# Performance work log

Measured on AMD Instinct MI355X. Metric: run time of the kernel, lower is better.

Reference implementation:

```python
import jax, jax.numpy as jnp
import numpy as np

B, S1, S2, S3, I, O = 4, 64, 64, 64, 32, 32
MX, MZ = 16, 16
HID = O * 2  # factor=2 feedforward hidden


def setup_inputs() -> dict:
    key = jax.random.key(0)
    ks = jax.random.split(key, 5)
    x = jax.random.normal(ks[0], (B, S1, S2, S3, I), jnp.float32)
    # xavier-normal-ish scale for complex fourier weights stored as [...,2]
    sw = np.float32(np.sqrt(2.0 / (I + O)))
    wx = jax.random.normal(ks[1], (I, O, MX, 2), jnp.float32) * sw
    wz = jax.random.normal(ks[2], (I, O, MZ, 2), jnp.float32) * sw
    w1 = jax.random.normal(ks[3], (O, HID), jnp.float32) * np.float32(np.sqrt(1.0 / O))
    b1 = jnp.zeros((HID,), jnp.float32)
    w2 = jax.random.normal(ks[4], (HID, O), jnp.float32) * np.float32(np.sqrt(1.0 / HID))
    b2 = jnp.zeros((O,), jnp.float32)
    return {"x": x, "wx": wx, "wz": wz, "w1": w1, "b1": b1, "w2": w2, "b2": b2}


def _forward_fourier(x, wx, wz):
    # x: [b, i, s1, s2, s3]
    # z-axis branch
    cwz = wz[..., 0] + 1j * wz[..., 1]          # [i, o, mz] complex
    xfz = jnp.fft.rfft(x, axis=-1, norm='ortho')  # [b,i,s1,s2,S3//2+1]
    pz = jnp.einsum('bixyz,ioz->boxyz', xfz[..., :MZ], cwz)
    pz = jnp.pad(pz, ((0, 0), (0, 0), (0, 0), (0, 0), (0, S3 // 2 + 1 - MZ)))
    xz = jnp.fft.irfft(pz, n=S3, axis=-1, norm='ortho')
    # x-axis branch (note: modes_y branch contributes 0 in the source, xy=0.0)
    cwx = wx[..., 0] + 1j * wx[..., 1]          # [i, o, mx]
    xfx = jnp.fft.rfft(x, axis=2, norm='ortho')  # [b,i,S1//2+1,s2,s3]
    px = jnp.einsum('bixyz,iox->boxyz', xfx[:, :, :MX], cwx)
    px = jnp.pad(px, ((0, 0), (0, 0), (0, S1 // 2 + 1 - MX), (0, 0), (0, 0)))
    xx = jnp.fft.irfft(px, n=S1, axis=2, norm='ortho')
    return xx + xz


def reference(x, wx, wz, w1, b1, w2, b2):
    xt = jnp.transpose(x, (0, 4, 1, 2, 3))      # b i s1 s2 s3
    y = _forward_fourier(xt, wx, wz)
    y = jnp.transpose(y, (0, 2, 3, 4, 1))       # b s1 s2 s3 o
    # backcast FeedForward: Linear -> ReLU -> Linear (dropout=0, no norms)
    h = jax.nn.relu(y @ w1 + b1)
    b_out = h @ w2 + b2
    return b_out
```

## Files before the change

### kernel.cpp

```cpp
#include <hip/hip_runtime.h>

namespace {

typedef _Float16 half_t;
typedef half_t f16x2 __attribute__((ext_vector_type(2)));
typedef half_t f16x8 __attribute__((ext_vector_type(8)));
typedef float f32x4 __attribute__((ext_vector_type(4)));

constexpr size_t RSTR = 64 * 64 * 32;

constexpr int WS_TF = 0;
constexpr int WS_TI = 2048;
constexpr int WS_WZ = 4096;
constexpr int WS_WX = 69632;
constexpr int WS_W1 = 135168;
constexpr int WS_W2 = 137216;

__device__ __forceinline__ float f4get(const float4& v, int u) {
  return u == 0 ? v.x : (u == 1 ? v.y : (u == 2 ? v.z : v.w));
}

__device__ __forceinline__ f32x4 mfma16(f16x8 a, f16x8 b, f32x4 c) {
  return __builtin_amdgcn_mfma_f32_16x16x32_f16(a, b, c, 0, 0, 0);
}

__global__ __launch_bounds__(256) void kinit(const float* __restrict__ wx,
                                             const float* __restrict__ wz,
                                             const float* __restrict__ w1,
                                             const float* __restrict__ w2,
                                             half_t* __restrict__ wsh) {
  const int id = blockIdx.x * 256 + threadIdx.x;
  const int l = id & 63, r = l & 15, g = l >> 4;
  f16x8 frag;
  if (id < 256) {
    int fid = id >> 6, mt = fid >> 1, kt = fid & 1;
#pragma unroll
    for (int e = 0; e < 8; ++e) {
      int k = kt * 32 + 8 * g + e;
      int mc = mt * 16 + r, m = mc >> 1, p = mc & 1;
      float s, c;
      sincospif((float)(m * k) * (1.0f / 32.0f), &s, &c);
      frag[e] = (half_t)(0.125f * (p ? -s : c));
    }
    *(f16x8*)(wsh + WS_TF + (size_t)id * 8) = frag;
  } else if (id < 512) {
    int id2 = id - 256, mt = id2 >> 6;
#pragma unroll
    for (int e = 0; e < 8; ++e) {
      int zp = mt * 16 + r;
      int k = 8 * g + e, m = k >> 1, p = k & 1;
      float s, c;
      sincospif((float)(m * zp) * (1.0f / 32.0f), &s, &c);
      float sc = (m == 0) ? 0.125f : 0.25f;
      frag[e] = (half_t)(p ? -sc * s : sc * c);
    }
    *(f16x8*)(wsh + WS_TI + (size_t)id2 * 8) = frag;
  } else if (id < 16896) {
    int id2 = id - 512;
    const float* wsrc = wz;
    size_t off = WS_WZ;
    if (id2 >= 8192) { id2 -= 8192; wsrc = wx; off = WS_WX; }
    int fid = id2 >> 6, m = fid >> 3, kt = (fid >> 2) & 1, nt = fid & 3;
#pragma unroll
    for (int e = 0; e < 8; ++e) {
      int k = kt * 32 + 8 * g + e, i = k >> 1, p = k & 1;
      int n = nt * 16 + r, o = n >> 1, q = n & 1;
      int base = ((i * 32 + o) * 16 + m) * 2;
      float re = wsrc[base], im = wsrc[base + 1];
      frag[e] = (half_t)(q ? (p ? re : im) : (p ? -im : re));
    }
    *(f16x8*)(wsh + off + (size_t)id2 * 8) = frag;
  } else if (id < 17152) {
    int id2 = id - 16896, nt = id2 >> 6;
#pragma unroll
    for (int e = 0; e < 8; ++e) {
      int k = 8 * g + e, n = nt * 16 + r;
      frag[e] = (half_t)w1[k * 64 + n];
    }
    *(f16x8*)(wsh + WS_W1 + (size_t)id2 * 8) = frag;
  } else if (id < 17408) {
    int id2 = id - 17152, fid = id2 >> 6, kt = fid >> 1, nt = fid & 1;
#pragma unroll
    for (int e = 0; e < 8; ++e) {
      int k = kt * 32 + 8 * g + e, n = nt * 16 + r;
      frag[e] = (half_t)w2[k * 32 + n];
    }
    *(f16x8*)(wsh + WS_W2 + (size_t)id2 * 8) = frag;
  }
}

template <int BR>
__global__ __launch_bounds__(256) void kspec(const float* __restrict__ x,
                                             const half_t* __restrict__ wsh,
                                             const float* __restrict__ b1g,
                                             const float* __restrict__ b2g,
                                             float* __restrict__ outf) {
  __shared__ __align__(16) char smraw[49152];
  half_t* XB = (half_t*)smraw;
  half_t* FB = (half_t*)smraw;
  half_t* PB = (half_t*)(smraw + 32768);
  half_t* outh = (half_t*)outf;
  const int t = threadIdx.x, l = t & 63, w = t >> 6, r = l & 15, g = l >> 4;
  const f32x4 vzero = {0.f, 0.f, 0.f, 0.f};

  const int col0 = blockIdx.x * 8;
  size_t xbase = (size_t)col0 * 2048, zstr = 32, cstr = 2048;

  {
    int c = t >> 5, sub = t & 31;
    int i4 = (sub & 7) * 4, zq = sub >> 3;
    const float* xp = x + xbase + (size_t)c * cstr + i4;
#pragma unroll
    for (int zo = 0; zo < 2; ++zo) {
      int zb = zq * 16 + zo * 8;
      float4 v[8];
#pragma unroll
      for (int zz = 0; zz < 8; ++zz)
        v[zz] = *(const float4*)(xp + (size_t)(zb + zz) * zstr);
#pragma unroll
      for (int u = 0; u < 4; ++u) {
        f16x8 rowv;
#pragma unroll
        for (int zz = 0; zz < 8; ++zz) rowv[zz] = (half_t)f4get(v[zz], u);
        int rowi = c * 32 + i4 + u;
        int gr = (zb >> 3) ^ (rowi & 7);
        *(f16x8*)(XB + rowi * 64 + gr * 8) = rowv;
      }
    }
  }
  __syncthreads();

  f32x4 fa[2][4];
#pragma unroll
  for (int mt = 0; mt < 2; ++mt)
#pragma unroll
    for (int nt = 0; nt < 4; ++nt) fa[mt][nt] = vzero;
  {
    f16x8 Atf[2][2], Bx[4][2];
#pragma unroll
    for (int mt = 0; mt < 2; ++mt)
#pragma unroll
      for (int kt = 0; kt < 2; ++kt)
        Atf[mt][kt] = *(const f16x8*)(wsh + WS_TF + (size_t)((mt * 2 + kt) * 64 + l) * 8);
#pragma unroll
    for (int nt = 0; nt < 4; ++nt)
#pragma unroll
      for (int kt = 0; kt < 2; ++kt) {
        int rowi = w * 64 + nt * 16 + r;
        int gr = (kt * 4 + g) ^ (rowi & 7);
        Bx[nt][kt] = *(const f16x8*)(XB + rowi * 64 + gr * 8);
      }
#pragma unroll
    for (int kt = 0; kt < 2; ++kt)
#pragma unroll
      for (int nt = 0; nt < 4; ++nt)
#pragma unroll
        for (int mt = 0; mt < 2; ++mt)
          fa[mt][nt] = mfma16(Atf[mt][kt], Bx[nt][kt], fa[mt][nt]);
  }
  __syncthreads();

#pragma unroll
  for (int mt = 0; mt < 2; ++mt)
#pragma unroll
    for (int nt = 0; nt < 4; ++nt)
#pragma unroll
      for (int q = 0; q < 4; ++q) {
        int mc = mt * 16 + 4 * g + q, m = mc >> 1, p = mc & 1;
        int n = w * 64 + nt * 16 + r, c = n >> 5, i = n & 31;
        int k = 2 * i + p;
        FB[(m * 16 + c) * 64 + ((k >> 3) ^ (c & 7)) * 8 + (k & 7)] = (half_t)fa[mt][nt][q];
      }
  __syncthreads();

  const half_t* WF = wsh + WS_WZ;
#pragma unroll
  for (int j = 0; j < 4; ++j) {
    int m = w * 4 + j;
    f16x8 Af[2];
#pragma unroll
    for (int kt = 0; kt < 2; ++kt) {
      int gr = (kt * 4 + g) ^ (r & 7);
      Af[kt] = *(const f16x8*)(FB + (m * 16 + r) * 64 + gr * 8);
    }
    f32x4 pa[4];
#pragma unroll
    for (int nt = 0; nt < 4; ++nt) pa[nt] = vzero;
#pragma unroll
    for (int kt = 0; kt < 2; ++kt)
#pragma unroll
      for (int nt = 0; nt < 4; ++nt) {
        f16x8 Bw = *(const f16x8*)(WF + (size_t)((m * 8 + kt * 4 + nt) * 64 + l) * 8);
        pa[nt] = mfma16(Af[kt], Bw, pa[nt]);
      }
#pragma unroll
    for (int nt = 0; nt < 4; ++nt)
#pragma unroll
      for (int q = 0; q < 4; ++q) {
        int c = 4 * g + q;
        if (c < 8) {
          int n = nt * 16 + r, o = n >> 1, q2 = n & 1;
          int k = 2 * m + q2;
          PB[(c * 32 + o) * 32 + ((k >> 3) ^ (o & 3)) * 8 + (k & 7)] = (half_t)pa[nt][q];
        }
      }
  }
  __syncthreads();

  {
    f16x8 Ati[4];
#pragma unroll
    for (int mt = 0; mt < 4; ++mt)
      Ati[mt] = *(const f16x8*)(wsh + WS_TI + (size_t)(mt * 64 + l) * 8);
#pragma unroll
    for (int cc = 0; cc < 2; ++cc) {
      int c = w * 2 + cc;
      f16x8 Bp[2];
#pragma unroll
      for (int nt = 0; nt < 2; ++nt) {
        int o = nt * 16 + r;
        Bp[nt] = *(const f16x8*)(PB + (c * 32 + o) * 32 + (g ^ (o & 3)) * 8);
      }
      f32x4 ya[4][2];
#pragma unroll
      for (int mt = 0; mt < 4; ++mt)
#pragma unroll
        for (int nt = 0; nt < 2; ++nt) ya[mt][nt] = mfma16(Ati[mt], Bp[nt], vzero);
#pragma unroll
      for (int mt = 0; mt < 4; ++mt)
#pragma unroll
        for (int nt = 0; nt < 2; ++nt)
#pragma unroll
          for (int q = 0; q < 4; ++q) {
            int zp = mt * 16 + 4 * g + q, o = nt * 16 + r;
            outh[(size_t)(col0 + c) * 4096 + zp * 64 + o] = (half_t)ya[mt][nt][q];
          }
    }
  }
}

__global__ __launch_bounds__(256, 4) void kx4(const float* __restrict__ x,
                                              const half_t* __restrict__ wsh,
                                              const float* __restrict__ b1g,
                                              const float* __restrict__ b2g,
                                              float* __restrict__ outf) {
  __shared__ __align__(16) half_t smh[16384];
  half_t* XB = smh;
  half_t* FB = smh + 8192;
  half_t* PB = smh + 12288;
  half_t* YL = smh;
  half_t* HL = smh + 8192;
  half_t* outh = (half_t*)outf;
  const int t = threadIdx.x, l = t & 63, w = t >> 6, r = l & 15, g = l >> 4;
  const f32x4 vzero = {0.f, 0.f, 0.f, 0.f};

  const int d = blockIdx.x;
  const int pp = (d & 7) * 512 + (d >> 3);
  const int col0 = pp * 4;
  const int b = col0 >> 12, s2 = (col0 >> 6) & 63, s30 = col0 & 63;
  const size_t xbase = (size_t)b * 8388608 + (size_t)s2 * 2048 + (size_t)s30 * 32;

  {
    int sub = t & 31, zq = t >> 5;
    int c = sub >> 3, i4 = (sub & 7) * 4;
    const float* xp = x + xbase + (size_t)c * 32 + i4 + (size_t)(zq * 8) * RSTR;
    float4 v[8];
#pragma unroll
    for (int zz = 0; zz < 8; ++zz) v[zz] = *(const float4*)(xp + (size_t)zz * RSTR);
#pragma unroll
    for (int uu = 0; uu < 4; ++uu) {
      int u = (uu + sub) & 3;
      f16x8 rowv;
#pragma unroll
      for (int zz = 0; zz < 8; ++zz) rowv[zz] = (half_t)f4get(v[zz], u);
      int rowi = c * 32 + i4 + u;
      *(f16x8*)(XB + rowi * 64 + (zq ^ (rowi & 7)) * 8) = rowv;
    }
  }
  __syncthreads();

  f32x4 fa[2][2];
  {
    f16x8 Atf[2][2], Bx[2][2];
#pragma unroll
    for (int mt = 0; mt < 2; ++mt)
#pragma unroll
      for (int kt = 0; kt < 2; ++kt)
        Atf[mt][kt] = *(const f16x8*)(wsh + WS_TF + (size_t)((mt * 2 + kt) * 64 + l) * 8);
#pragma unroll
    for (int nt = 0; nt < 2; ++nt)
#pragma unroll
      for (int kt = 0; kt < 2; ++kt) {
        int rowi = w * 32 + nt * 16 + r;
        Bx[nt][kt] = *(const f16x8*)(XB + rowi * 64 + (((kt * 4 + g) ^ (rowi & 7))) * 8);
      }
#pragma unroll
    for (int mt = 0; mt < 2; ++mt)
#pragma unroll
      for (int nt = 0; nt < 2; ++nt) fa[mt][nt] = vzero;
#pragma unroll
    for (int kt = 0; kt < 2; ++kt)
#pragma unroll
      for (int nt = 0; nt < 2; ++nt)
#pragma unroll
        for (int mt = 0; mt < 2; ++mt)
          fa[mt][nt] = mfma16(Atf[mt][kt], Bx[nt][kt], fa[mt][nt]);
  }
#pragma unroll
  for (int mt = 0; mt < 2; ++mt)
#pragma unroll
    for (int nt = 0; nt < 2; ++nt)
#pragma unroll
      for (int pr = 0; pr < 2; ++pr) {
        int q = 2 * pr;
        int mc = mt * 16 + 4 * g + q, m = mc >> 1;
        int n = w * 32 + nt * 16 + r, c = n >> 5, i = n & 31;
        int k = 2 * i;
        f16x2 pairv = {(half_t)fa[mt][nt][q], (half_t)fa[mt][nt][q + 1]};
        *(f16x2*)(FB + (m * 4 + c) * 64 + (((k >> 3) ^ ((m + 2 * c) & 7))) * 8 + (k & 7)) =
            pairv;
      }
  __syncthreads();

#pragma unroll
  for (int j = 0; j < 4; ++j) {
    int m = w * 4 + j;
    int rsel = r & 3, keym = (m + 2 * rsel) & 7;
    f16x8 Af[2];
#pragma unroll
    for (int kt = 0; kt < 2; ++kt)
      Af[kt] = *(const f16x8*)(FB + (m * 4 + rsel) * 64 + (((kt * 4 + g) ^ keym)) * 8);
    f32x4 pa[4];
#pragma unroll
    for (int nt = 0; nt < 4; ++nt) pa[nt] = vzero;
#pragma unroll
    for (int kt = 0; kt < 2; ++kt)
#pragma unroll
      for (int nt = 0; nt < 4; ++nt) {
        f16x8 Bw = *(const f16x8*)(wsh + WS_WX + (size_t)((m * 8 + kt * 4 + nt) * 64 + l) * 8);
        pa[nt] = mfma16(Af[kt], Bw, pa[nt]);
      }
    if (g == 0) {
#pragma unroll
      for (int nt = 0; nt < 4; ++nt)
#pragma unroll
        for (int q = 0; q < 4; ++q) {
          int c = q;
          int n = nt * 16 + r, o = n >> 1, q2 = n & 1;
          int k = 2 * m + q2;
          PB[(c * 32 + o) * 32 + (((k >> 3) ^ (o & 3))) * 8 + (k & 7)] = (half_t)pa[nt][q];
        }
    }
  }
  __syncthreads();

  f16x8 Ati[4];
#pragma unroll
  for (int mt = 0; mt < 4; ++mt)
    Ati[mt] = *(const f16x8*)(wsh + WS_TI + (size_t)(mt * 64 + l) * 8);
  f16x8 Bp[2];
#pragma unroll
  for (int nt = 0; nt < 2; ++nt) {
    int o = nt * 16 + r;
    Bp[nt] = *(const f16x8*)(PB + (w * 32 + o) * 32 + ((g ^ (o & 3))) * 8);
  }
  f16x8 yzf[2][2];
#pragma unroll
  for (int rr = 0; rr < 2; ++rr)
#pragma unroll
    for (int mt = 0; mt < 2; ++mt) {
      int rowA = rr * 128 + w * 32 + mt * 16 + r;
      int zp = rowA & 63, c = rowA >> 6;
      size_t col = (size_t)b * 4096 + (size_t)zp * 64 + s2;
      yzf[rr][mt] = *(const f16x8*)(outh + col * 4096 + (size_t)(s30 + c) * 64 + 8 * g);
    }
  f16x8 W1F[4];
#pragma unroll
  for (int nt = 0; nt < 4; ++nt)
    W1F[nt] = *(const f16x8*)(wsh + WS_W1 + (size_t)(nt * 64 + l) * 8);
  float b1v[4];
#pragma unroll
  for (int nt = 0; nt < 4; ++nt) b1v[nt] = b1g[nt * 16 + r];
  {
    f32x4 ya[4][2];
#pragma unroll
    for (int mt = 0; mt < 4; ++mt)
#pragma unroll
      for (int nt = 0; nt < 2; ++nt) ya[mt][nt] = mfma16(Ati[mt], Bp[nt], vzero);
#pragma unroll
    for (int mt = 0; mt < 4; ++mt)
#pragma unroll
      for (int nt = 0; nt < 2; ++nt)
#pragma unroll
        for (int q = 0; q < 4; ++q) {
          int zp = mt * 16 + 4 * g + q, o = nt * 16 + r;
          int rowi = w * 64 + zp;
          YL[rowi * 32 + (((o >> 3) ^ ((rowi >> 2) & 3))) * 8 + (o & 7)] =
              (half_t)ya[mt][nt][q];
        }
  }
  __syncthreads();

  f16x8 W2F[4];
#pragma unroll
  for (int f = 0; f < 4; ++f)
    W2F[f] = *(const f16x8*)(wsh + WS_W2 + (size_t)(f * 64 + l) * 8);
  float b2v[2];
#pragma unroll
  for (int nt = 0; nt < 2; ++nt) b2v[nt] = b2g[nt * 16 + r];

  for (int rr = 0; rr < 2; ++rr) {
    f16x8 AY[2];
#pragma unroll
    for (int mt = 0; mt < 2; ++mt) {
      int rowA = rr * 128 + w * 32 + mt * 16 + r;
      f16x8 ay = *(const f16x8*)(YL + rowA * 32 + ((g ^ ((rowA >> 2) & 3))) * 8);
      AY[mt] = ay + yzf[rr][mt];
    }
    f32x4 ha[2][4];
#pragma unroll
    for (int mt = 0; mt < 2; ++mt)
#pragma unroll
      for (int nt = 0; nt < 4; ++nt) ha[mt][nt] = mfma16(AY[mt], W1F[nt], vzero);
#pragma unroll
    for (int mt = 0; mt < 2; ++mt)
#pragma unroll
      for (int nt = 0; nt < 4; ++nt)
#pragma unroll
        for (int q = 0; q < 4; ++q) {
          int rloc = w * 32 + mt * 16 + 4 * g + q, n = nt * 16 + r;
          float hv = fmaxf(ha[mt][nt][q] + b1v[nt], 0.f);
          HL[rloc * 64 + (((n >> 3) ^ ((rloc >> 2) & 7))) * 8 + (n & 7)] = (half_t)hv;
        }
    __syncthreads();
    f16x8 AH[2][2];
#pragma unroll
    for (int mt = 0; mt < 2; ++mt)
#pragma unroll
      for (int kt = 0; kt < 2; ++kt) {
        int rowA2 = w * 32 + mt * 16 + r;
        AH[mt][kt] =
            *(const f16x8*)(HL + rowA2 * 64 + (((kt * 4 + g) ^ ((rowA2 >> 2) & 7))) * 8);
      }
    f32x4 oa[2][2];
#pragma unroll
    for (int mt = 0; mt < 2; ++mt)
#pragma unroll
      for (int nt = 0; nt < 2; ++nt) oa[mt][nt] = vzero;
#pragma unroll
    for (int kt = 0; kt < 2; ++kt)
#pragma unroll
      for (int mt = 0; mt < 2; ++mt)
#pragma unroll
        for (int nt = 0; nt < 2; ++nt)
          oa[mt][nt] = mfma16(AH[mt][kt], W2F[kt * 2 + nt], oa[mt][nt]);
#pragma unroll
    for (int mt = 0; mt < 2; ++mt)
#pragma unroll
      for (int nt = 0; nt < 2; ++nt)
#pragma unroll
        for (int q = 0; q < 4; ++q) {
          int rowg = rr * 128 + w * 32 + mt * 16 + 4 * g + q;
          int c = rowg >> 6, zp = rowg & 63, o = nt * 16 + r;
          outf[(size_t)b * 8388608 + (size_t)zp * RSTR + (size_t)s2 * 2048 +
               (size_t)(s30 + c) * 32 + o] = oa[mt][nt][q] + b2v[nt];
        }
    if (rr == 0) __syncthreads();
  }
}

}

extern "C" void kernel_launch(void* const* d_in, const int* in_sizes, int n_in,
                              void* d_out, int out_size, void* d_ws, size_t ws_size,
                              hipStream_t stream) {
  const float* x = (const float*)d_in[0];
  const float* wx = (const float*)d_in[1];
  const float* wz = (const float*)d_in[2];
  const float* w1 = (const float*)d_in[3];
  const float* b1 = (const float*)d_in[4];
  const float* w2 = (const float*)d_in[5];
  const float* b2 = (const float*)d_in[6];
  float* out = (float*)d_out;
  half_t* wsh = (half_t*)d_ws;

  hipLaunchKernelGGL(kinit, dim3(68), dim3(256), 0, stream, wx, wz, w1, w2, wsh);
  hipLaunchKernelGGL((kspec<0>), dim3(2048), dim3(256), 0, stream, x, wsh, b1, b2, out);
  hipLaunchKernelGGL(kx4, dim3(4096), dim3(256), 0, stream, x, wsh, b1, b2, out);
}
```

Baseline: 134.1 us.

## Reorder z-branch intermediate layout so consumer kernel reads contiguous chunks

The z-axis spectral kernel now assigns blocks to (batch, s1-pair, s2-quad) tiles and writes its half-precision intermediate in a permuted layout indexed by s1 and s3 parity. The x-axis kernel reads that intermediate with a matching new address formula. The goal is to make the cross-kernel intermediate loads in the consumer, and possibly the producer's stores, more coalesced and local. The risk is a mismatch between the two index mappings, plus a scattered store pattern in the producer.

```diff
diff --git a/kernel.cpp b/kernel.cpp
--- a/kernel.cpp
+++ b/kernel.cpp
@@ -15,6 +15,7 @@
 constexpr int WS_WX = 69632;
 constexpr int WS_W1 = 135168;
 constexpr int WS_W2 = 137216;
+
 
 __device__ __forceinline__ float f4get(const float4& v, int u) {
   return u == 0 ? v.x : (u == 1 ? v.y : (u == 2 ? v.z : v.w));
@@ -89,12 +90,9 @@
   }
 }
 
-template <int BR>
-__global__ __launch_bounds__(256) void kspec(const float* __restrict__ x,
-                                             const half_t* __restrict__ wsh,
-                                             const float* __restrict__ b1g,
-                                             const float* __restrict__ b2g,
-                                             float* __restrict__ outf) {
+__global__ __launch_bounds__(256) void kz(const float* __restrict__ x,
+                                          const half_t* __restrict__ wsh,
+                                          float* __restrict__ outf) {
   __shared__ __align__(16) char smraw[49152];
   half_t* XB = (half_t*)smraw;
   half_t* FB = (half_t*)smraw;
@@ -103,20 +101,24 @@
   const int t = threadIdx.x, l = t & 63, w = t >> 6, r = l & 15, g = l >> 4;
   const f32x4 vzero = {0.f, 0.f, 0.f, 0.f};
 
-  const int col0 = blockIdx.x * 8;
-  size_t xbase = (size_t)col0 * 2048, zstr = 32, cstr = 2048;
+  const int d = blockIdx.x;
+  const int bb = d >> 9;
+  const int s1base = 2 * ((d >> 4) & 31);
+  const int s2base = 4 * (d & 15);
+  const int K = s1base >> 1;
 
   {
     int c = t >> 5, sub = t & 31;
     int i4 = (sub & 7) * 4, zq = sub >> 3;
-    const float* xp = x + xbase + (size_t)c * cstr + i4;
+    int s1c = s1base + (c >> 2), s2c = s2base + (c & 3);
+    const float* xp = x + (size_t)((bb * 64 + s1c) * 64 + s2c) * 2048 + i4;
 #pragma unroll
     for (int zo = 0; zo < 2; ++zo) {
       int zb = zq * 16 + zo * 8;
       float4 v[8];
 #pragma unroll
       for (int zz = 0; zz < 8; ++zz)
-        v[zz] = *(const float4*)(xp + (size_t)(zb + zz) * zstr);
+        v[zz] = *(const float4*)(xp + (size_t)(zb + zz) * 32);
 #pragma unroll
       for (int u = 0; u < 4; ++u) {
         f16x8 rowv;
@@ -215,6 +217,7 @@
 #pragma unroll
     for (int cc = 0; cc < 2; ++cc) {
       int c = w * 2 + cc;
+      int z = c >> 2, s2c = s2base + (c & 3);
       f16x8 Bp[2];
 #pragma unroll
       for (int nt = 0; nt < 2; ++nt) {
@@ -226,14 +229,17 @@
       for (int mt = 0; mt < 4; ++mt)
 #pragma unroll
         for (int nt = 0; nt < 2; ++nt) ya[mt][nt] = mfma16(Ati[mt], Bp[nt], vzero);
+      const size_t cbase = (size_t)bb * 16777216 + (size_t)s2c * 4096 + z * 32;
 #pragma unroll
       for (int mt = 0; mt < 4; ++mt)
 #pragma unroll
         for (int nt = 0; nt < 2; ++nt)
 #pragma unroll
           for (int q = 0; q < 4; ++q) {
-            int zp = mt * 16 + 4 * g + q, o = nt * 16 + r;
-            outh[(size_t)(col0 + c) * 4096 + zp * 64 + o] = (half_t)ya[mt][nt][q];
+            int s3 = mt * 16 + 4 * g + q, o = nt * 16 + r;
+            outh[cbase + (size_t)((s3 & 1) * 32 + K) * 262144 +
+                 (size_t)((s3 >> 2) * 4 + ((s3 >> 1) & 1)) * 64 + o] =
+                (half_t)ya[mt][nt][q];
           }
     }
   }
@@ -250,7 +256,7 @@
   half_t* PB = smh + 12288;
   half_t* YL = smh;
   half_t* HL = smh + 8192;
-  half_t* outh = (half_t*)outf;
+  const half_t* outh = (const half_t*)outf;
   const int t = threadIdx.x, l = t & 63, w = t >> 6, r = l & 15, g = l >> 4;
   const f32x4 vzero = {0.f, 0.f, 0.f, 0.f};
 
@@ -369,10 +375,10 @@
   for (int rr = 0; rr < 2; ++rr)
 #pragma unroll
     for (int mt = 0; mt < 2; ++mt) {
-      int rowA = rr * 128 + w * 32 + mt * 16 + r;
-      int zp = rowA & 63, c = rowA >> 6;
-      size_t col = (size_t)b * 4096 + (size_t)zp * 64 + s2;
-      yzf[rr][mt] = *(const f16x8*)(outh + col * 4096 + (size_t)(s30 + c) * 64 + 8 * g);
+      size_t addr = (size_t)b * 16777216 +
+                    (size_t)((w >> 1) * 32 + (w & 1) * 16 + mt * 8 + (r >> 1)) * 262144 +
+                    (size_t)s2 * 4096 + (size_t)(s30 + rr) * 64 + (r & 1) * 32 + 8 * g;
+      yzf[rr][mt] = *(const f16x8*)(outh + addr);
     }
   f16x8 W1F[4];
 #pragma unroll
@@ -485,6 +491,6 @@
   half_t* wsh = (half_t*)d_ws;
 
   hipLaunchKernelGGL(kinit, dim3(68), dim3(256), 0, stream, wx, wz, w1, w2, wsh);
-  hipLaunchKernelGGL((kspec<0>), dim3(2048), dim3(256), 0, stream, x, wsh, b1, b2, out);
+  hipLaunchKernelGGL(kz, dim3(2048), dim3(256), 0, stream, x, wsh, out);
   hipLaunchKernelGGL(kx4, dim3(4096), dim3(256), 0, stream, x, wsh, b1, b2, out);
 }
```

Measured after the change: 122.4 us. 8.7% less time.
